# Performance work log

Measured on AMD Instinct MI355X. Metric: run time of the kernel, lower is better.

Reference implementation:

```python
import jax, jax.numpy as jnp
import numpy as np

NUM_HEADS = 16
FOCUS = 3.0
EPS = 1e-6


def setup_inputs() -> dict:
    key = jax.random.key(0)
    ks = jax.random.split(key, 6)
    B, N, C = 8, 4096, 1024
    x = jax.random.normal(ks[0], (B, N, C), dtype=jnp.float32)
    scale = jax.random.normal(ks[1], (1, 1, C), dtype=jnp.float32) * 0.02
    pos_enc = jax.random.normal(ks[2], (1, N, C), dtype=jnp.float32) * 0.02
    qkv_w = jax.random.normal(ks[3], (3 * C, C), dtype=jnp.float32) * (C ** -0.5)
    proj_w = jax.random.normal(ks[4], (C, C), dtype=jnp.float32) * (C ** -0.5)
    proj_b = jnp.zeros((C,), dtype=jnp.float32)
    return {"x": x, "scale": scale, "pos_enc": pos_enc, "qkv_w": qkv_w,
            "proj_w": proj_w, "proj_b": proj_b}


def reference(x, scale, pos_enc, qkv_w, proj_w, proj_b):
    B, N, C = x.shape
    h = NUM_HEADS
    # qkv projection (no bias)
    qkv = jnp.einsum('bnc,dc->bnd', x, qkv_w).reshape(B, N, 3, C)
    q, k, v = qkv[:, :, 0], qkv[:, :, 1], qkv[:, :, 2]
    k = k + pos_enc
    sc = jax.nn.softplus(scale)  # (1,1,C)
    q = jax.nn.relu(q) + EPS
    k = jax.nn.relu(k) + EPS
    q = q / sc
    k = k / sc
    q_norm = jnp.linalg.norm(q, axis=-1, keepdims=True)
    k_norm = jnp.linalg.norm(k, axis=-1, keepdims=True)
    # focusing_factor = 3 <= 6 branch
    q = q ** FOCUS
    k = k ** FOCUS
    q = q / jnp.linalg.norm(q, axis=-1, keepdims=True) * q_norm
    k = k / jnp.linalg.norm(k, axis=-1, keepdims=True) * k_norm
    # split heads: b n (h c) -> (b h) n c
    def split_heads(t):
        return t.reshape(B, N, h, C // h).transpose(0, 2, 1, 3).reshape(B * h, N, C // h)
    q, k, v = split_heads(q), split_heads(k), split_heads(v)
    q = q.astype(jnp.float32); k = k.astype(jnp.float32); v = v.astype(jnp.float32)
    z = 1.0 / (jnp.einsum('bic,bc->bi', q, k.sum(axis=1)) + EPS)  # (bh, N)
    # kv-first linear attention path (i*j*(c+d) > c*d*(i+j) for these shapes)
    kv = jnp.einsum('bjc,bjd->bcd', k, v)  # (bh, c, d)
    o = jnp.einsum('bic,bcd,bi->bid', q, kv, z)
    # merge heads: (b h) n c -> b n (h c)
    o = o.reshape(B, h, N, C // h).transpose(0, 2, 1, 3).reshape(B, N, C)
    o = jnp.einsum('bnc,dc->bnd', o, proj_w) + proj_b
    return o
```

## Files before the change

kernel.cpp:

```cpp
#include <hip/hip_runtime.h>
#include <hip/hip_bf16.h>
#include <cstdint>
#include <cstddef>


typedef __bf16 bf16;
typedef __bf16 bf16x4 __attribute__((ext_vector_type(4)));
typedef __bf16 bf16x8 __attribute__((ext_vector_type(8)));
typedef float f32x4 __attribute__((ext_vector_type(4)));
typedef float f32x2 __attribute__((ext_vector_type(2)));

#define NB 8
#define NSEQ 4096
#define NC 1024
#define NH 16
#define ND 64
#define NBH 128
#define NM 32768
#define EPSF 1e-6f
#define KSPLIT 8

__device__ __forceinline__ void async16(const void* g, void* l) {
  __builtin_amdgcn_global_load_lds(
      (const __attribute__((address_space(1))) void*)g,
      (__attribute__((address_space(3))) void*)l, 16, 0, 0);
}

__device__ __forceinline__ unsigned pack_bf16(float a, float b) {
  union { bf16 h[2]; unsigned u; } t;
  t.h[0] = (bf16)a; t.h[1] = (bf16)b;
  return t.u;
}

#define BAR() asm volatile("s_barrier" ::: "memory")
#define WAIT_LGKM(N) asm volatile("s_waitcnt lgkmcnt(" #N ")" ::: "memory")
#define WAIT_VM(N) asm volatile("s_waitcnt vmcnt(" #N ")" ::: "memory")
#define SCHEDB() __builtin_amdgcn_sched_barrier(0)

__global__ __launch_bounds__(256) void cvt_bf16(const float* __restrict__ src,
                                                bf16* __restrict__ dst, int n4) {
  int i = blockIdx.x * 256 + threadIdx.x;
  if (i < n4) {
    f32x4 v = ((const f32x4*)src)[i];
    bf16x4 o;
    o[0] = (bf16)v[0]; o[1] = (bf16)v[1]; o[2] = (bf16)v[2]; o[3] = (bf16)v[3];
    ((bf16x4*)dst)[i] = o;
  }
}

__global__ __launch_bounds__(256) void prep_scale(const float* __restrict__ scale,
                                                  float* __restrict__ inv_sc) {
  int c = blockIdx.x * 256 + threadIdx.x;
  if (c < NC) inv_sc[c] = 1.0f / log1pf(expf(scale[c]));
}

template <int MODE>
__global__ __launch_bounds__(512, 2) void gemm_bt8(const bf16* __restrict__ A,
                                                   const bf16* __restrict__ Bm, int K,
                                                   bf16* __restrict__ outqk,
                                                   bf16* __restrict__ outv,
                                                   float* __restrict__ outf,
                                                   const float* __restrict__ bias) {
  __shared__ bf16 As[2 * 16384];
  __shared__ bf16 Bs[2 * 16384];

  const int tid = threadIdx.x;
  const int w = tid >> 6, lane = tid & 63;
  const int q4 = lane >> 4, l16 = lane & 15;
  const int l7 = l16 & 7;
  const int wm = (w >> 2) * 128, wn = (w & 3) * 64;

  const int gx = gridDim.x;
  const int nwg = gx * gridDim.y;
  const int bid0 = blockIdx.y * gx + blockIdx.x;
  const int cpx = nwg >> 3;
  const int bid = (bid0 & 7) * cpx + (bid0 >> 3);
  const long row0 = (long)(bid / gx) * 256;
  const long col0 = (long)(bid % gx) * 256;

  const int s0 = w * 128 + lane;
  const int ra = s0 >> 3;
  const int cg = ((s0 & 7) ^ (ra & 7)) << 3;
  const int dl = s0 << 3;

  const bf16* Abase = A + (row0 + ra) * (long)K + cg;
  const bf16* Bbase = Bm + (col0 + ra) * (long)K + cg;
  const long rstep = 8 * (long)K;
  const long hstep = 128 * (long)K;

  auto stA = [&](int buf, int h, int k0) {
    const bf16* g = Abase + h * hstep + k0;
    bf16* l = As + buf * 16384 + h * 8192 + dl;
    async16(g, l);
    async16(g + rstep, l + 512);
  };
  auto stB = [&](int buf, int h, int k0) {
    const bf16* g = Bbase + h * hstep + k0;
    bf16* l = Bs + buf * 16384 + h * 8192 + dl;
    async16(g, l);
    async16(g + rstep, l + 512);
  };

  const int nkt = K >> 6;

  stA(0, 0, 0); stA(0, 1, 0);
  stB(0, 0, 0); stB(0, 1, 0);
  {
    const int k1p = (nkt > 1 ? 1 : 0) << 6;
    stB(1, 0, k1p); stB(1, 1, k1p);
  }
  WAIT_VM(4);
  BAR();

  f32x4 acc[8][4] = {};
  bf16x8 af[4][2], bfr[4][2];

  for (int t = 0; t < nkt; ++t) {
    const int p = t & 1, q = p ^ 1;
    const int pb = p * 16384;
    const int k1 = (t + 1 < nkt ? t + 1 : nkt - 1) << 6;
    const int k2 = (t + 2 < nkt ? t + 2 : nkt - 1) << 6;

#pragma unroll
    for (int mi = 0; mi < 4; mi++) {
      const int rb = (wm + mi * 16 + l16) * 64;
#pragma unroll
      for (int ks = 0; ks < 2; ks++)
        af[mi][ks] = *(const bf16x8*)&As[pb + rb + (((ks * 4 + q4) ^ l7) << 3)];
    }
#pragma unroll
    for (int ni = 0; ni < 2; ni++) {
      const int rb = (wn + ni * 16 + l16) * 64;
#pragma unroll
      for (int ks = 0; ks < 2; ks++)
        bfr[ni][ks] = *(const bf16x8*)&Bs[pb + rb + (((ks * 4 + q4) ^ l7) << 3)];
    }
    stA(q, 0, k1);
    WAIT_LGKM(8);
    BAR();
    WAIT_LGKM(0); SCHEDB();
    __builtin_amdgcn_s_setprio(1);
#pragma unroll
    for (int mi = 0; mi < 4; mi++)
#pragma unroll
      for (int ni = 0; ni < 2; ni++)
#pragma unroll
        for (int ks = 0; ks < 2; ks++)
          acc[mi][ni] = __builtin_amdgcn_mfma_f32_16x16x32_bf16(
              af[mi][ks], bfr[ni][ks], acc[mi][ni], 0, 0, 0);
    __builtin_amdgcn_s_setprio(0);
    BAR();

#pragma unroll
    for (int ni = 2; ni < 4; ni++) {
      const int rb = (wn + ni * 16 + l16) * 64;
#pragma unroll
      for (int ks = 0; ks < 2; ks++)
        bfr[ni][ks] = *(const bf16x8*)&Bs[pb + rb + (((ks * 4 + q4) ^ l7) << 3)];
    }
    stA(q, 1, k1);
    BAR();
    WAIT_LGKM(0); SCHEDB();
    __builtin_amdgcn_s_setprio(1);
#pragma unroll
    for (int mi = 0; mi < 4; mi++)
#pragma unroll
      for (int ni = 2; ni < 4; ni++)
#pragma unroll
        for (int ks = 0; ks < 2; ks++)
          acc[mi][ni] = __builtin_amdgcn_mfma_f32_16x16x32_bf16(
              af[mi][ks], bfr[ni][ks], acc[mi][ni], 0, 0, 0);
    __builtin_amdgcn_s_setprio(0);
    BAR();

#pragma unroll
    for (int mi = 0; mi < 4; mi++) {
      const int rb = (wm + 64 + mi * 16 + l16) * 64;
#pragma unroll
      for (int ks = 0; ks < 2; ks++)
        af[mi][ks] = *(const bf16x8*)&As[pb + rb + (((ks * 4 + q4) ^ l7) << 3)];
    }
    stB(p, 0, k2);
    BAR();
    WAIT_LGKM(0); SCHEDB();
    __builtin_amdgcn_s_setprio(1);
#pragma unroll
    for (int mi = 0; mi < 4; mi++)
#pragma unroll
      for (int ni = 0; ni < 2; ni++)
#pragma unroll
        for (int ks = 0; ks < 2; ks++)
          acc[4 + mi][ni] = __builtin_amdgcn_mfma_f32_16x16x32_bf16(
              af[mi][ks], bfr[ni][ks], acc[4 + mi][ni], 0, 0, 0);
    __builtin_amdgcn_s_setprio(0);
    BAR();

    stB(p, 1, k2);
    BAR();
    __builtin_amdgcn_s_setprio(1);
#pragma unroll
    for (int mi = 0; mi < 4; mi++)
#pragma unroll
      for (int ni = 2; ni < 4; ni++)
#pragma unroll
        for (int ks = 0; ks < 2; ks++)
          acc[4 + mi][ni] = __builtin_amdgcn_mfma_f32_16x16x32_bf16(
              af[mi][ks], bfr[ni][ks], acc[4 + mi][ni], 0, 0, 0);
    __builtin_amdgcn_s_setprio(0);
    WAIT_VM(4);
    BAR();
  }
  WAIT_VM(0);

  const int ev = (l16 & 1) == 0;
#pragma unroll
  for (int mi = 0; mi < 8; mi++) {
    long gr0 = row0 + wm + mi * 16 + q4 * 4;
#pragma unroll
    for (int ni = 0; ni < 4; ni++) {
      long gc = col0 + wn + ni * 16 + l16;
      long cb = gc & ~1L;
      long r2 = gr0 + (ev ? 0 : 2);
      if (MODE == 0) {
        unsigned m01 = pack_bf16(acc[mi][ni][0], acc[mi][ni][1]);
        unsigned m23 = pack_bf16(acc[mi][ni][2], acc[mi][ni][3]);
        unsigned p01 = __shfl_xor(m01, 1);
        unsigned p23 = __shfl_xor(m23, 1);
        unsigned xs = ev ? m01 : p23;
        unsigned ys = ev ? p01 : m23;
        unsigned da = (xs & 0xFFFFu) | (ys << 16);
        unsigned db = (xs >> 16) | (ys & 0xFFFF0000u);
        if (col0 < 2048) {
          *(unsigned*)(outqk + r2 * 2048 + cb) = da;
          *(unsigned*)(outqk + (r2 + 1) * 2048 + cb) = db;
        } else {
          *(unsigned*)(outv + r2 * 1024 + (cb - 2048)) = da;
          *(unsigned*)(outv + (r2 + 1) * 1024 + (cb - 2048)) = db;
        }
      } else {
        float bsum = bias[gc];
        float v0 = acc[mi][ni][0] + bsum, v1 = acc[mi][ni][1] + bsum;
        float v2 = acc[mi][ni][2] + bsum, v3 = acc[mi][ni][3] + bsum;
        float p0 = __shfl_xor(v0, 1), p1 = __shfl_xor(v1, 1);
        float p2 = __shfl_xor(v2, 1), p3 = __shfl_xor(v3, 1);
        f32x2 sa, sb;
        sa[0] = ev ? v0 : p2; sa[1] = ev ? p0 : v2;
        sb[0] = ev ? v1 : p3; sb[1] = ev ? p1 : v3;
        *(f32x2*)(outf + r2 * 1024 + cb) = sa;
        *(f32x2*)(outf + (r2 + 1) * 1024 + cb) = sb;
      }
    }
  }
}

__global__ __launch_bounds__(256) void transform_qk(const bf16* __restrict__ qkb,
                                                    const bf16* __restrict__ peb,
                                                    const float* __restrict__ inv_sc,
                                                    bf16* __restrict__ qp,
                                                    bf16* __restrict__ kp) {
  __shared__ f32x4 red[4];
  const long row = blockIdx.x;
  const int n = (int)(row & (NSEQ - 1));
  const int c0 = threadIdx.x * 4;

  bf16x4 qb = *(const bf16x4*)(qkb + row * 2048 + c0);
  bf16x4 kb = *(const bf16x4*)(qkb + row * 2048 + 1024 + c0);
  bf16x4 pe = *(const bf16x4*)(peb + (long)n * 1024 + c0);
  f32x4 isc = *(const f32x4*)(inv_sc + c0);

  f32x4 q3, k3;
  float s2q = 0, s6q = 0, s2k = 0, s6k = 0;
#pragma unroll
  for (int j = 0; j < 4; j++) {
    float qv = (fmaxf((float)qb[j], 0.f) + EPSF) * isc[j];
    float kv = (fmaxf((float)kb[j] + (float)pe[j], 0.f) + EPSF) * isc[j];
    float q3v = qv * qv * qv, k3v = kv * kv * kv;
    q3[j] = q3v; k3[j] = k3v;
    s2q += qv * qv; s6q += q3v * q3v;
    s2k += kv * kv; s6k += k3v * k3v;
  }
  f32x4 s; s[0] = s2q; s[1] = s6q; s[2] = s2k; s[3] = s6k;
#pragma unroll
  for (int off = 32; off > 0; off >>= 1) {
    s[0] += __shfl_xor(s[0], off);
    s[1] += __shfl_xor(s[1], off);
    s[2] += __shfl_xor(s[2], off);
    s[3] += __shfl_xor(s[3], off);
  }
  const int wv = threadIdx.x >> 6;
  if ((threadIdx.x & 63) == 0) red[wv] = s;
  __syncthreads();
  f32x4 tot = red[0] + red[1] + red[2] + red[3];
  float fq = sqrtf(tot[0] / tot[1]);
  float fk = sqrtf(tot[2] / tot[3]);

  bf16x4 qo, ko;
#pragma unroll
  for (int j = 0; j < 4; j++) {
    qo[j] = (bf16)(q3[j] * fq);
    ko[j] = (bf16)(k3[j] * fk);
  }
  *(bf16x4*)(qp + row * 1024 + c0) = qo;
  *(bf16x4*)(kp + row * 1024 + c0) = ko;
}

__global__ __launch_bounds__(256) void kv_partial(const bf16* __restrict__ kp,
                                                  const bf16* __restrict__ vb,
                                                  float* __restrict__ kv_part,
                                                  float* __restrict__ ks_part) {
  __shared__ float kls[64 * 64];
  __shared__ float vls[64 * 64];
  const int sp = blockIdx.x;
  const int bh = blockIdx.y;
  const int b = bh >> 4, h = bh & 15;
  const int tid = threadIdx.x;
  const int c0 = (tid & 15) * 4, d0 = (tid >> 4) * 4;

  f32x4 acc4[4] = {};
  float ks[4] = {0.f, 0.f, 0.f, 0.f};

  for (int chunk = 0; chunk < NSEQ / KSPLIT / 64; ++chunk) {
    const int n0 = sp * (NSEQ / KSPLIT) + chunk * 64;
    __syncthreads();
    for (int it = tid; it < 1024; it += 256) {
      int nn = it >> 4, cc = (it & 15) * 4;
      long g = ((long)(b * NSEQ + n0 + nn)) * NC + h * ND + cc;
      bf16x4 kb = *(const bf16x4*)(kp + g);
      bf16x4 vv = *(const bf16x4*)(vb + g);
      f32x4 kf, vf;
#pragma unroll
      for (int j = 0; j < 4; j++) { kf[j] = (float)kb[j]; vf[j] = (float)vv[j]; }
      *(f32x4*)&kls[nn * 64 + cc] = kf;
      *(f32x4*)&vls[nn * 64 + cc] = vf;
    }
    __syncthreads();
    for (int nn = 0; nn < 64; ++nn) {
      f32x4 kk = *(const f32x4*)&kls[nn * 64 + c0];
      f32x4 vv = *(const f32x4*)&vls[nn * 64 + d0];
#pragma unroll
      for (int i = 0; i < 4; i++) acc4[i] += kk[i] * vv;
      if (tid < 16) {
#pragma unroll
        for (int i = 0; i < 4; i++) ks[i] += kk[i];
      }
    }
  }
  const long base = ((long)(sp * NBH + bh)) * 4096;
#pragma unroll
  for (int i = 0; i < 4; i++)
    *(f32x4*)&kv_part[base + (c0 + i) * 64 + d0] = acc4[i];
  if (tid < 16) {
#pragma unroll
    for (int i = 0; i < 4; i++)
      ks_part[(long)(sp * NBH + bh) * 64 + c0 + i] = ks[i];
  }
}

__global__ __launch_bounds__(256) void reduce_parts(const float* __restrict__ src,
                                                    float* __restrict__ dst, int n) {
  int i = blockIdx.x * 256 + threadIdx.x;
  if (i < n) {
    float s = 0.f;
    for (int p = 0; p < KSPLIT; ++p) s += src[(long)p * n + i];
    dst[i] = s;
  }
}

__global__ __launch_bounds__(256) void z_o(const bf16* __restrict__ qp,
                                           const float* __restrict__ kvm,
                                           const float* __restrict__ ksum,
                                           bf16* __restrict__ ob) {
  __shared__ float kvs[4096];
  __shared__ float kss[64];
  const int bh = blockIdx.x >> 4, chunk = blockIdx.x & 15;
  const int b = bh >> 4, h = bh & 15;
  const int tid = threadIdx.x;

  for (int i = tid; i < 1024; i += 256)
    *(f32x4*)&kvs[i * 4] = *(const f32x4*)&kvm[(long)bh * 4096 + i * 4];
  if (tid < 16)
    *(f32x4*)&kss[tid * 4] = *(const f32x4*)&ksum[(long)bh * 64 + tid * 4];
  __syncthreads();

  const int i = chunk * 256 + tid;
  const bf16* qrow = qp + ((long)(b * NSEQ + i)) * NC + h * ND;

  float s = 0.f;
#pragma unroll
  for (int c8 = 0; c8 < 8; ++c8) {
    bf16x8 q8 = *(const bf16x8*)(qrow + c8 * 8);
#pragma unroll
    for (int j = 0; j < 8; j++) s += (float)q8[j] * kss[c8 * 8 + j];
  }
  const float z = 1.0f / (s + EPSF);

  f32x4 o4[16] = {};
  for (int c8 = 0; c8 < 8; ++c8) {
    bf16x8 q8 = *(const bf16x8*)(qrow + c8 * 8);
#pragma unroll
    for (int j = 0; j < 8; j++) {
      float qc = (float)q8[j];
      const f32x4* kr = (const f32x4*)&kvs[(c8 * 8 + j) * 64];
#pragma unroll
      for (int d4 = 0; d4 < 16; ++d4) o4[d4] += qc * kr[d4];
    }
  }
  bf16* orow = ob + ((long)(b * NSEQ + i)) * NC + h * ND;
#pragma unroll
  for (int d4 = 0; d4 < 16; ++d4) {
    bf16x4 o;
#pragma unroll
    for (int j = 0; j < 4; j++) o[j] = (bf16)(o4[d4][j] * z);
    *(bf16x4*)(orow + d4 * 4) = o;
  }
}

extern "C" void kernel_launch(void* const* d_in, const int* in_sizes, int n_in,
                              void* d_out, int out_size, void* d_ws, size_t ws_size,
                              hipStream_t stream) {
  const float* x = (const float*)d_in[0];
  const float* scale = (const float*)d_in[1];
  const float* pos_enc = (const float*)d_in[2];
  const float* qkv_w = (const float*)d_in[3];
  const float* proj_w = (const float*)d_in[4];
  const float* proj_b = (const float*)d_in[5];
  float* out = (float*)d_out;

  char* ws = (char*)d_ws;
  size_t off = 0;
  auto alloc = [&](size_t bytes) {
    char* p = ws + off;
    off += (bytes + 255) & ~(size_t)255;
    return p;
  };
  bf16* xb = (bf16*)alloc((size_t)NM * NC * 2);
  bf16* wqkv = (bf16*)alloc((size_t)3 * NC * NC * 2);
  bf16* wproj = (bf16*)alloc((size_t)NC * NC * 2);
  float* inv_sc = (float*)alloc(NC * 4);
  bf16* peb = (bf16*)alloc((size_t)NSEQ * NC * 2);
  bf16* vb = (bf16*)alloc((size_t)NM * NC * 2);
  bf16* kp = (bf16*)alloc((size_t)NM * NC * 2);
  float* ks_part = (float*)alloc((size_t)KSPLIT * NBH * ND * 4);
  float* ksum = (float*)alloc((size_t)NBH * ND * 4);
  float* kvm = (float*)alloc((size_t)NBH * ND * ND * 4);
  bf16* qkb = (bf16*)alloc((size_t)NM * 2048 * 2);
  (void)ws_size; (void)n_in; (void)in_sizes; (void)out_size;

  bf16* ob = (bf16*)qkb;
  float* kv_part = (float*)((char*)qkb + (size_t)NM * NC * 2);
  bf16* qp = xb;

  cvt_bf16<<<dim3((NM * NC / 4 + 255) / 256), 256, 0, stream>>>(x, xb, NM * NC / 4);
  cvt_bf16<<<dim3((3 * NC * NC / 4 + 255) / 256), 256, 0, stream>>>(qkv_w, wqkv, 3 * NC * NC / 4);
  cvt_bf16<<<dim3((NC * NC / 4 + 255) / 256), 256, 0, stream>>>(proj_w, wproj, NC * NC / 4);
  cvt_bf16<<<dim3((NSEQ * NC / 4 + 255) / 256), 256, 0, stream>>>(pos_enc, peb, NSEQ * NC / 4);
  prep_scale<<<dim3(4), 256, 0, stream>>>(scale, inv_sc);

  gemm_bt8<0><<<dim3(12, 128), 512, 0, stream>>>(xb, wqkv, NC, qkb, vb, nullptr, nullptr);

  transform_qk<<<dim3(NM), 256, 0, stream>>>(qkb, peb, inv_sc, qp, kp);

  kv_partial<<<dim3(KSPLIT, NBH), 256, 0, stream>>>(kp, vb, kv_part, ks_part);
  reduce_parts<<<dim3((NBH * ND + 255) / 256), 256, 0, stream>>>(ks_part, ksum, NBH * ND);
  reduce_parts<<<dim3((NBH * 4096 + 255) / 256), 256, 0, stream>>>(kv_part, kvm, NBH * 4096);

  z_o<<<dim3(NBH * 16), 256, 0, stream>>>(qp, kvm, ksum, ob);

  gemm_bt8<1><<<dim3(4, 128), 512, 0, stream>>>(ob, wproj, NC, nullptr, nullptr, out, proj_b);
}
```

Measured before the change: 816.6 us.

## Compute K^T V with bf16 MFMA and retile z_o to four rows per thread

The kv_partial kernel is replaced by kv_mfma. It stages K and V transposed as bf16 in LDS with an XOR swizzle, computes the 64x64 K^T V partials with 16x16x32 bf16 MFMA instructions, and gets the K column sums from an MFMA against a vector of ones. The z_o kernel is retiled so each thread handles 4 rows and 16 output columns, which reuses each kv LDS read across rows and folds the z dot product into the same loop. The costs targeted are scalar FMA throughput in the kv stage and redundant LDS reads in the output stage. The trade-offs are scalar byte-wide transposed LDS stores and bf16 MFMA inputs, which match the bf16 precision already used for kp and vb.

```diff
diff --git a/kernel.cpp b/kernel.cpp
--- a/kernel.cpp
+++ b/kernel.cpp
@@ -304,55 +304,71 @@
   *(bf16x4*)(kp + row * 1024 + c0) = ko;
 }
 
-__global__ __launch_bounds__(256) void kv_partial(const bf16* __restrict__ kp,
-                                                  const bf16* __restrict__ vb,
-                                                  float* __restrict__ kv_part,
-                                                  float* __restrict__ ks_part) {
-  __shared__ float kls[64 * 64];
-  __shared__ float vls[64 * 64];
+__global__ __launch_bounds__(256) void kv_mfma(const bf16* __restrict__ kp,
+                                               const bf16* __restrict__ vb,
+                                               float* __restrict__ kv_part,
+                                               float* __restrict__ ks_part) {
+  __shared__ bf16 kT[64 * 64];
+  __shared__ bf16 vT[64 * 64];
   const int sp = blockIdx.x;
   const int bh = blockIdx.y;
   const int b = bh >> 4, h = bh & 15;
   const int tid = threadIdx.x;
-  const int c0 = (tid & 15) * 4, d0 = (tid >> 4) * 4;
-
-  f32x4 acc4[4] = {};
-  float ks[4] = {0.f, 0.f, 0.f, 0.f};
+  const int w = tid >> 6, lane = tid & 63;
+  const int q4 = lane >> 4, l16 = lane & 15;
+  const int nn = tid >> 2, cg = (tid & 3) * 16;
+
+  f32x4 acc[4] = {};
+  f32x4 aks = {};
+  bf16x8 ones;
+#pragma unroll
+  for (int j = 0; j < 8; j++) ones[j] = (bf16)1.0f;
 
   for (int chunk = 0; chunk < NSEQ / KSPLIT / 64; ++chunk) {
     const int n0 = sp * (NSEQ / KSPLIT) + chunk * 64;
     __syncthreads();
-    for (int it = tid; it < 1024; it += 256) {
-      int nn = it >> 4, cc = (it & 15) * 4;
-      long g = ((long)(b * NSEQ + n0 + nn)) * NC + h * ND + cc;
-      bf16x4 kb = *(const bf16x4*)(kp + g);
-      bf16x4 vv = *(const bf16x4*)(vb + g);
-      f32x4 kf, vf;
-#pragma unroll
-      for (int j = 0; j < 4; j++) { kf[j] = (float)kb[j]; vf[j] = (float)vv[j]; }
-      *(f32x4*)&kls[nn * 64 + cc] = kf;
-      *(f32x4*)&vls[nn * 64 + cc] = vf;
+    {
+      const long g = ((long)(b * NSEQ + n0 + nn)) * NC + h * ND + cg;
+      bf16x8 k0 = *(const bf16x8*)(kp + g);
+      bf16x8 k1 = *(const bf16x8*)(kp + g + 8);
+      bf16x8 v0 = *(const bf16x8*)(vb + g);
+      bf16x8 v1 = *(const bf16x8*)(vb + g + 8);
+#pragma unroll
+      for (int j = 0; j < 8; j++) {
+        const int c = cg + j;
+        const int idx = c * 64 + (((nn >> 3) ^ (c & 7)) << 3) + (nn & 7);
+        kT[idx] = k0[j]; vT[idx] = v0[j];
+        const int c2 = cg + 8 + j;
+        const int idx2 = c2 * 64 + (((nn >> 3) ^ (c2 & 7)) << 3) + (nn & 7);
+        kT[idx2] = k1[j]; vT[idx2] = v1[j];
+      }
     }
     __syncthreads();
-    for (int nn = 0; nn < 64; ++nn) {
-      f32x4 kk = *(const f32x4*)&kls[nn * 64 + c0];
-      f32x4 vv = *(const f32x4*)&vls[nn * 64 + d0];
-#pragma unroll
-      for (int i = 0; i < 4; i++) acc4[i] += kk[i] * vv;
-      if (tid < 16) {
-#pragma unroll
-        for (int i = 0; i < 4; i++) ks[i] += kk[i];
+#pragma unroll
+    for (int kk = 0; kk < 2; kk++) {
+      const int cA = w * 16 + l16;
+      bf16x8 af = *(const bf16x8*)&kT[cA * 64 + (((kk * 4 + q4) ^ (cA & 7)) << 3)];
+#pragma unroll
+      for (int dt = 0; dt < 4; dt++) {
+        const int dR = dt * 16 + l16;
+        bf16x8 bf_ = *(const bf16x8*)&vT[dR * 64 + (((kk * 4 + q4) ^ (dR & 7)) << 3)];
+        acc[dt] = __builtin_amdgcn_mfma_f32_16x16x32_bf16(af, bf_, acc[dt], 0, 0, 0);
       }
+      aks = __builtin_amdgcn_mfma_f32_16x16x32_bf16(af, ones, aks, 0, 0, 0);
     }
   }
   const long base = ((long)(sp * NBH + bh)) * 4096;
-#pragma unroll
-  for (int i = 0; i < 4; i++)
-    *(f32x4*)&kv_part[base + (c0 + i) * 64 + d0] = acc4[i];
-  if (tid < 16) {
-#pragma unroll
-    for (int i = 0; i < 4; i++)
-      ks_part[(long)(sp * NBH + bh) * 64 + c0 + i] = ks[i];
+  const int c0 = w * 16 + q4 * 4;
+#pragma unroll
+  for (int ri = 0; ri < 4; ri++) {
+#pragma unroll
+    for (int dt = 0; dt < 4; dt++)
+      kv_part[base + (long)(c0 + ri) * 64 + dt * 16 + l16] = acc[dt][ri];
+  }
+  if (l16 == 0) {
+#pragma unroll
+    for (int ri = 0; ri < 4; ri++)
+      ks_part[(long)(sp * NBH + bh) * 64 + c0 + ri] = aks[ri];
   }
 }
 
@@ -375,6 +391,8 @@
   const int bh = blockIdx.x >> 4, chunk = blockIdx.x & 15;
   const int b = bh >> 4, h = bh & 15;
   const int tid = threadIdx.x;
+  const int rg = tid >> 2;
+  const int qd = (tid & 3) * 16;
 
   for (int i = tid; i < 1024; i += 256)
     *(f32x4*)&kvs[i * 4] = *(const f32x4*)&kvm[(long)bh * 4096 + i * 4];
@@ -382,36 +400,41 @@
     *(f32x4*)&kss[tid * 4] = *(const f32x4*)&ksum[(long)bh * 64 + tid * 4];
   __syncthreads();
 
-  const int i = chunk * 256 + tid;
-  const bf16* qrow = qp + ((long)(b * NSEQ + i)) * NC + h * ND;
-
-  float s = 0.f;
-#pragma unroll
+  const long i0 = (long)b * NSEQ + chunk * 256 + rg * 4;
+  const bf16* q0 = qp + i0 * NC + h * ND;
+
+  f32x4 o4[4][4] = {};
+  float s[4] = {0.f, 0.f, 0.f, 0.f};
   for (int c8 = 0; c8 < 8; ++c8) {
-    bf16x8 q8 = *(const bf16x8*)(qrow + c8 * 8);
-#pragma unroll
-    for (int j = 0; j < 8; j++) s += (float)q8[j] * kss[c8 * 8 + j];
-  }
-  const float z = 1.0f / (s + EPSF);
-
-  f32x4 o4[16] = {};
-  for (int c8 = 0; c8 < 8; ++c8) {
-    bf16x8 q8 = *(const bf16x8*)(qrow + c8 * 8);
+    bf16x8 q8[4];
+#pragma unroll
+    for (int r = 0; r < 4; r++) q8[r] = *(const bf16x8*)(q0 + r * NC + c8 * 8);
 #pragma unroll
     for (int j = 0; j < 8; j++) {
-      float qc = (float)q8[j];
-      const f32x4* kr = (const f32x4*)&kvs[(c8 * 8 + j) * 64];
-#pragma unroll
-      for (int d4 = 0; d4 < 16; ++d4) o4[d4] += qc * kr[d4];
-    }
-  }
-  bf16* orow = ob + ((long)(b * NSEQ + i)) * NC + h * ND;
-#pragma unroll
-  for (int d4 = 0; d4 < 16; ++d4) {
-    bf16x4 o;
-#pragma unroll
-    for (int j = 0; j < 4; j++) o[j] = (bf16)(o4[d4][j] * z);
-    *(bf16x4*)(orow + d4 * 4) = o;
+      const int c = c8 * 8 + j;
+      const f32x4* kr = (const f32x4*)&kvs[c * 64 + qd];
+      const f32x4 k0 = kr[0], k1 = kr[1], k2 = kr[2], k3 = kr[3];
+      const float ksc = kss[c];
+#pragma unroll
+      for (int r = 0; r < 4; r++) {
+        const float qc = (float)q8[r][j];
+        o4[r][0] += qc * k0; o4[r][1] += qc * k1;
+        o4[r][2] += qc * k2; o4[r][3] += qc * k3;
+        s[r] += qc * ksc;
+      }
+    }
+  }
+#pragma unroll
+  for (int r = 0; r < 4; r++) {
+    const float z = 1.0f / (s[r] + EPSF);
+    bf16* orow = ob + (i0 + r) * NC + h * ND + qd;
+#pragma unroll
+    for (int d4 = 0; d4 < 4; d4++) {
+      bf16x4 o;
+#pragma unroll
+      for (int j = 0; j < 4; j++) o[j] = (bf16)(o4[r][d4][j] * z);
+      *(bf16x4*)(orow + d4 * 4) = o;
+    }
   }
 }
 
@@ -460,7 +483,7 @@
 
   transform_qk<<<dim3(NM), 256, 0, stream>>>(qkb, peb, inv_sc, qp, kp);
 
-  kv_partial<<<dim3(KSPLIT, NBH), 256, 0, stream>>>(kp, vb, kv_part, ks_part);
+  kv_mfma<<<dim3(KSPLIT, NBH), 256, 0, stream>>>(kp, vb, kv_part, ks_part);
   reduce_parts<<<dim3((NBH * ND + 255) / 256), 256, 0, stream>>>(ks_part, ksum, NBH * ND);
   reduce_parts<<<dim3((NBH * 4096 + 255) / 256), 256, 0, stream>>>(kv_part, kvm, NBH * 4096);
 
```

After: 750.2 us. -8.1%, faster.
